# Optimization experiments

Measured on AMD Instinct MI355X. Metric: run time of the kernel, lower is better.

The kernel has to match this reference:

```python
import jax, jax.numpy as jnp
import numpy as np

MEM = 64  # memory_size from init_kwargs


def setup_inputs() -> dict:
    key = jax.random.key(0)
    ks = jax.random.split(key, 16)
    D, H, B, T = 128, 512, 512, 128
    n = lambda k, shape, s=0.02: jax.random.normal(k, shape, dtype=jnp.float32) * s
    # Gate order for stacked weights: [s, f, i, T, u, o]; Ws stacks [f, i, T, u, o].
    return {
        "X_seq": n(ks[0], (B, T, D + 1), 1.0),
        "Wh": n(ks[1], (6, H, H)), "bh_lin": jnp.zeros((6, H)),
        "Wx": n(ks[2], (6, D, H)), "bx_lin": jnp.zeros((6, H)),
        "Wst": n(ks[3], (1, H)), "bst": jnp.zeros((H,)),
        "Ws": n(ks[4], (5, H, H)), "bs_lin": jnp.zeros((5, H)),
        "bg": jnp.zeros((6, H)),
        "Waq": n(ks[5], (2 * H, H)), "baq": jnp.zeros((H,)),
        "Wah": n(ks[6], (H, H)), "bah": jnp.zeros((H,)),
        "vt": n(ks[7], (H, 1), 0.05),
        "W_h": n(ks[8], (H, H)), "b_Wh": jnp.zeros((H,)),
        "We": n(ks[9], (H, H)), "b_We": jnp.zeros((H,)),
        "Wg": n(ks[10], (D, H)), "b_Wg": jnp.zeros((H,)),
        "bh_p": jnp.zeros((H,)),
        "Wc": n(ks[11], (H, 1)), "bc": jnp.zeros((1,)),
    }


def reference(X_seq, Wh, bh_lin, Wx, bx_lin, Wst, bst, Ws, bs_lin, bg,
              Waq, baq, Wah, bah, vt, W_h, b_Wh, We, b_We, Wg, b_Wg, bh_p, Wc, bc):
    B, T, _ = X_seq.shape
    H = Wh.shape[-1]
    x_all = X_seq[:, :, :-1]          # [B, T, D]
    dt_all = X_seq[:, :, -1:]         # [B, T, 1]

    def step(carry, inp):
        h_prev, c_prev = carry
        x_t, d_t = inp                 # [B, D], [B, 1]
        # batched GEMMs over the 6 gates (s, f, i, T, u, o)
        pre_h = jnp.einsum('bh,ghk->gbk', h_prev, Wh) + bh_lin[:, None, :]
        pre_x = jnp.einsum('bd,gdk->gbk', x_t, Wx) + bx_lin[:, None, :]
        s_t = jnp.tanh(pre_h[0] + pre_x[0] + d_t @ Wst + bst + bg[0])
        pre_s = jnp.einsum('bh,ghk->gbk', s_t, Ws) + bs_lin[:, None, :]  # [f,i,T,u,o]
        f_t = jax.nn.sigmoid(pre_h[1] + pre_x[1] + pre_s[0] + bg[1])
        i_t = jax.nn.sigmoid(pre_h[2] + pre_x[2] + pre_s[1] + bg[2])
        T_t = jax.nn.sigmoid(pre_h[3] + pre_x[3] + pre_s[2] + bg[3])
        z_t = jnp.tanh(pre_h[4] + pre_x[4] + pre_s[3] + bg[4])
        c_t = f_t * c_prev + i_t * z_t + T_t * s_t
        o_t = jax.nn.sigmoid(pre_h[5] + pre_x[5] + pre_s[4] + bg[5])
        h_t = o_t * jnp.tanh(c_t)
        return (h_t, c_t), h_t

    h0 = jnp.zeros((B, H), dtype=X_seq.dtype)
    c0 = jnp.zeros((B, H), dtype=X_seq.dtype)
    xs = (jnp.swapaxes(x_all, 0, 1), jnp.swapaxes(dt_all, 0, 1))
    (h_last, c_last), h_tildes = jax.lax.scan(step, (h0, c0), xs)  # h_tildes: [T, B, H]

    # sliding window of last MEM hidden states (T >= MEM so all zeros are pushed out)
    hs = jnp.swapaxes(h_tildes[-MEM:], 0, 1)  # [B, MEM, H]

    q = jnp.concatenate([h_last, c_last], axis=1)                       # [B, 2H]
    o_att = jnp.tanh((q @ Waq + baq)[:, None, :] + hs @ Wah + bah)       # [B, MEM, H]
    alpha = jnp.exp((o_att @ vt)[..., 0])                                # [B, MEM] (matches torch exp/sum)
    alpha = alpha / jnp.sum(alpha, axis=1, keepdims=True)
    e_t = jnp.einsum('bm,bmh->bh', alpha, hs)
    h_fin = jnp.tanh(h_last @ W_h + b_Wh + e_t @ We + b_We
                     + x_all[:, -1] @ Wg + b_Wg + bh_p)
    return jax.nn.sigmoid(h_fin @ Wc + bc)  # [B, 1]
```

## Files before the change

### kernel.cpp

```cpp
#include <hip/hip_runtime.h>
#include <hip/hip_bf16.h>

typedef __bf16 bf16x8 __attribute__((ext_vector_type(8)));
typedef float f32x4 __attribute__((ext_vector_type(4)));

constexpr int NB   = 512;
constexpr int NT   = 128;
constexpr int ND   = 128;
constexpr int NH   = 512;
constexpr int NMEM = 64;
constexpr int KKA  = 640;
constexpr int KKB  = 1152;

constexpr int BAR_CNT = 0;
constexpr int BAR_GB  = 64;
constexpr int BAR_MFL = 8448;
constexpr int BAR_DFL = 12800;
constexpr int BAR_TOT = 16384;

__device__ __forceinline__ float sigm_(float x) { return 1.f / (1.f + expf(-x)); }

__device__ __forceinline__ unsigned ld_rlx_sys(const unsigned* p) {
    return __hip_atomic_load(p, __ATOMIC_RELAXED, __HIP_MEMORY_SCOPE_SYSTEM);
}
__device__ __forceinline__ unsigned ld_acq_sys(const unsigned* p) {
    return __hip_atomic_load(p, __ATOMIC_ACQUIRE, __HIP_MEMORY_SCOPE_SYSTEM);
}
__device__ __forceinline__ void st_rel_sys(unsigned* p, unsigned v) {
    __hip_atomic_store(p, v, __ATOMIC_RELEASE, __HIP_MEMORY_SCOPE_SYSTEM);
}
__device__ __forceinline__ unsigned ld_rlx_agt(const unsigned* p) {
    return __hip_atomic_load(p, __ATOMIC_RELAXED, __HIP_MEMORY_SCOPE_AGENT);
}
__device__ __forceinline__ unsigned ld_acq_agt(const unsigned* p) {
    return __hip_atomic_load(p, __ATOMIC_ACQUIRE, __HIP_MEMORY_SCOPE_AGENT);
}
__device__ __forceinline__ void st_rlx_agt(unsigned* p, unsigned v) {
    __hip_atomic_store(p, v, __ATOMIC_RELAXED, __HIP_MEMORY_SCOPE_AGENT);
}


__global__ void k_shufA(const float* __restrict__ Wh, const float* __restrict__ Wx,
                        __hip_bfloat16* __restrict__ WA_shuf) {
    int nb = blockIdx.x / 20, kk = blockIdx.x % 20;
    int lane = threadIdx.x;
    int n = nb * 16 + (lane & 15);
    int kbase = kk * 32 + (lane >> 4) * 8;
    size_t o = ((size_t)blockIdx.x * 64 + lane) * 8;
    for (int e = 0; e < 8; ++e) {
        int k = kbase + e;
        float v = (k < 512) ? Wh[(size_t)k * NH + n]
                            : Wx[(size_t)(k - 512) * NH + n];
        WA_shuf[o + e] = __float2bfloat16(v);
    }
}

__global__ void k_shufB(const float* __restrict__ Wh, const float* __restrict__ Wx,
                        const float* __restrict__ Ws, __hip_bfloat16* __restrict__ WB_shuf) {
    int idx = blockIdx.x;
    int kk = idx % 36, g = (idx / 36) % 5, jb = idx / 180;
    int lane = threadIdx.x;
    int j = jb * 16 + (lane & 15);
    int kbase = kk * 32 + (lane >> 4) * 8;
    size_t o = ((size_t)idx * 64 + lane) * 8;
    for (int e = 0; e < 8; ++e) {
        int k = kbase + e;
        float v;
        if (k < 512)      v = Wh[(size_t)(g + 1) * NH * NH + (size_t)k * NH + j];
        else if (k < 640) v = Wx[(size_t)(g + 1) * ND * NH + (size_t)(k - 512) * NH + j];
        else              v = Ws[(size_t)g * NH * NH + (size_t)(k - 640) * NH + j];
        WB_shuf[o + e] = __float2bfloat16(v);
    }
}

__global__ void k_shufW(const float* __restrict__ Wah, __hip_bfloat16* __restrict__ Wah_shuf) {
    int nb = blockIdx.x / 16, kk = blockIdx.x % 16;
    int lane = threadIdx.x;
    int j = nb * 16 + (lane & 15);
    int kbase = kk * 32 + (lane >> 4) * 8;
    size_t o = ((size_t)blockIdx.x * 64 + lane) * 8;
    for (int e = 0; e < 8; ++e)
        Wah_shuf[o + e] = __float2bfloat16(Wah[(size_t)(kbase + e) * NH + j]);
}

__global__ void k_biases(const float* bh_lin, const float* bx_lin, const float* bst,
                         const float* bs_lin, const float* bg,
                         const float* b_Wh, const float* b_We, const float* b_Wg, const float* bh_p,
                         float* bias_s, float* bias_g, float* bias_fin) {
    int j = threadIdx.x;
    bias_s[j] = bh_lin[j] + bx_lin[j] + bst[j] + bg[j];
    for (int g = 0; g < 5; ++g)
        bias_g[g * NH + j] = bh_lin[(g + 1) * NH + j] + bx_lin[(g + 1) * NH + j] +
                             bs_lin[g * NH + j] + bg[(g + 1) * NH + j];
    bias_fin[j] = b_Wh[j] + b_We[j] + b_Wg[j] + bh_p[j];
}

__global__ void k_init(const float* __restrict__ X_seq, float* __restrict__ Dt,
                       __hip_bfloat16* __restrict__ A_big, unsigned* __restrict__ bar) {
    int b = blockIdx.x, tid = threadIdx.x;
    if (b == 0) for (int i = tid; i < BAR_TOT; i += 256) bar[i] = 0;
    if (tid < NT) Dt[tid * NB + b] = X_seq[((size_t)b * NT + tid) * (ND + 1) + ND];
    for (int c = tid; c < KKB; c += 256) {
        float v = 0.f;
        if (c >= 512 && c < 640) v = X_seq[(size_t)b * NT * (ND + 1) + (c - 512)];
        A_big[(size_t)b * KKB + c] = __float2bfloat16(v);
    }
}

__device__ __forceinline__ void gbar2(unsigned* __restrict__ gb, int wg, unsigned gen) {
    __syncthreads();
    const int tid = threadIdx.x;
    if (tid == 0) st_rel_sys(&gb[wg * 32], gen);
    if (wg == 0) {
        while (ld_rlx_sys(&gb[tid * 32]) < gen) {}
        (void)ld_acq_sys(&gb[tid * 32]);
        __syncthreads();
        if (tid == 0) st_rel_sys(&gb[256 * 32], gen);
    }
    if (tid == 0) {
        while (ld_rlx_sys(&gb[256 * 32]) < gen) {}
        (void)ld_acq_sys(&gb[256 * 32]);
    }
    __syncthreads();
}

__device__ __forceinline__ void gbarL(unsigned* __restrict__ bar, unsigned xcd, unsigned rank,
                                      unsigned gen) {
    const int tid = threadIdx.x;
    __syncthreads();
    if (tid == 0) st_rlx_agt(&bar[BAR_MFL + (xcd * 32 + rank) * 16], gen);
    if (rank == 0) {
        if (tid < 32) { while (ld_rlx_agt(&bar[BAR_MFL + (xcd * 32 + tid) * 16]) < gen) {} }
        __syncthreads();
        if (tid == 0) st_rlx_agt(&bar[BAR_DFL + xcd * 32], gen);
    }
    if (tid == 0) {
        while (ld_rlx_agt(&bar[BAR_DFL + xcd * 32]) < gen) {}
        (void)ld_acq_agt(&bar[BAR_DFL + xcd * 32]);
    }
    __syncthreads();
}


__global__ __launch_bounds__(256, 1) void lstm_coop(
    const float* __restrict__ X_seq, const float* __restrict__ Dt,
    const __hip_bfloat16* __restrict__ WA_shuf, const __hip_bfloat16* __restrict__ WB_shuf,
    const float* __restrict__ bias_s, const float* __restrict__ bias_g,
    const float* __restrict__ Wst,
    __hip_bfloat16* __restrict__ A_big,
    float* __restrict__ c_last, float* __restrict__ s_f32, float* __restrict__ h_last,
    __hip_bfloat16* __restrict__ hist,
    unsigned* __restrict__ bar)
{
    const int wg = blockIdx.x;
    const int tid = threadIdx.x;
    const int wv = tid >> 6;
    const int lane = tid & 63;
    const int l15 = lane & 15, lhi = lane >> 4;

    __shared__ unsigned sh_meta[2];
    __shared__ unsigned sh_cnt[8];
    if (tid == 0) {
        unsigned xcc;
        asm volatile("s_getreg_b32 %0, hwreg(HW_REG_XCC_ID)" : "=s"(xcc));
        xcc &= 7u;
        unsigned r = __hip_atomic_fetch_add(&bar[BAR_CNT + xcc], 1u,
                                            __ATOMIC_RELAXED, __HIP_MEMORY_SCOPE_AGENT);
        sh_meta[0] = xcc; sh_meta[1] = r;
    }
    __syncthreads();
    gbar2(bar + BAR_GB, wg, 1u);
    if (tid < 8) sh_cnt[tid] = ld_rlx_sys(&bar[BAR_CNT + tid]);
    __syncthreads();
    bool local_ok = true;
    #pragma unroll
    for (int j = 0; j < 8; ++j) if (sh_cnt[j] != 32u) local_ok = false;

    const unsigned xcd  = local_ok ? sh_meta[0] : (unsigned)(wg & 7);
    const unsigned rank = local_ok ? sh_meta[1] : (unsigned)(wg >> 3);
    const int row_base  = (int)xcd * 64;

    const int colj = (int)rank * 16 + l15;

    const float ebs  = bias_s[colj];
    const float ewst = Wst[colj];
    float bgc[5];
    #pragma unroll
    for (int g = 0; g < 5; ++g) bgc[g] = bias_g[g * NH + colj];

    const __hip_bfloat16* wa_base = WA_shuf + (size_t)rank * 20 * 512 + lane * 8;
    const __hip_bfloat16* wb_base = WB_shuf + (size_t)rank * 5 * 36 * 512 + lane * 8;

    f32x4 c_reg = {0.f, 0.f, 0.f, 0.f};

    for (int t = 0; t < NT; ++t) {
        const int buf = t & 1;
        const __hip_bfloat16* A = A_big + (size_t)buf * NB * KKB;
        __hip_bfloat16* An = A_big + (size_t)(buf ^ 1) * NB * KKB;
        __hip_bfloat16* Aw = A_big + (size_t)buf * NB * KKB;

        {
            f32x4 acc = {0.f, 0.f, 0.f, 0.f};
            const __hip_bfloat16* arow = A + (size_t)(row_base + wv * 16 + l15) * KKB + lhi * 8;
            #pragma unroll 4
            for (int kk = 0; kk < 20; ++kk) {
                bf16x8 af = *reinterpret_cast<const bf16x8*>(arow + kk * 32);
                bf16x8 bfv = *reinterpret_cast<const bf16x8*>(wa_base + kk * 512);
                acc = __builtin_amdgcn_mfma_f32_16x16x32_bf16(af, bfv, acc, 0, 0, 0);
            }
            #pragma unroll
            for (int r = 0; r < 4; ++r) {
                int row = row_base + wv * 16 + lhi * 4 + r;
                float s = tanhf(acc[r] + ebs + Dt[t * NB + row] * ewst);
                s_f32[row * NH + colj] = s;
                Aw[(size_t)row * KKB + 640 + colj] = __float2bfloat16(s);
            }
        }
        if (local_ok) gbarL(bar, xcd, rank, (unsigned)(2 * t + 1));
        else          gbar2(bar + BAR_GB, wg, (unsigned)(2 * t + 2));

        {
            f32x4 acc[5] = {};
            const __hip_bfloat16* arow = A + (size_t)(row_base + wv * 16 + l15) * KKB + lhi * 8;
            for (int kk = 0; kk < 36; ++kk) {
                bf16x8 af = *reinterpret_cast<const bf16x8*>(arow + kk * 32);
                #pragma unroll
                for (int g = 0; g < 5; ++g) {
                    bf16x8 bfv = *reinterpret_cast<const bf16x8*>(wb_base + (g * 36 + kk) * 512);
                    acc[g] = __builtin_amdgcn_mfma_f32_16x16x32_bf16(af, bfv, acc[g], 0, 0, 0);
                }
            }
            #pragma unroll
            for (int r = 0; r < 4; ++r) {
                int row = row_base + wv * 16 + lhi * 4 + r;
                float f  = sigm_(acc[0][r] + bgc[0]);
                float i  = sigm_(acc[1][r] + bgc[1]);
                float Tg = sigm_(acc[2][r] + bgc[2]);
                float z  = tanhf(acc[3][r] + bgc[3]);
                float o  = sigm_(acc[4][r] + bgc[4]);
                float sv = s_f32[row * NH + colj];
                float cn = f * c_reg[r] + i * z + Tg * sv;
                c_reg[r] = cn;
                float hn = o * tanhf(cn);
                An[(size_t)row * KKB + colj] = __float2bfloat16(hn);
                if (t >= NT - NMEM)
                    hist[((size_t)(t - (NT - NMEM)) * NB + row) * NH + colj] = __float2bfloat16(hn);
                if (t == NT - 1) {
                    h_last[row * NH + colj] = hn;
                    c_last[row * NH + colj] = cn;
                }
            }
            if (t < NT - 1) {
                int idx = (int)rank * 256 + tid;
                int rr = idx >> 7, d = idx & 127;
                int row = row_base + rr;
                float xv = X_seq[((size_t)row * NT + (t + 1)) * (ND + 1) + d];
                An[(size_t)row * KKB + 512 + d] = __float2bfloat16(xv);
            }
        }
        if (local_ok) gbarL(bar, xcd, rank, (unsigned)(2 * t + 2));
        else          gbar2(bar + BAR_GB, wg, (unsigned)(2 * t + 3));
    }
}


__global__ void k_qa(const float* __restrict__ h_last, const float* __restrict__ c_last,
                     const float* __restrict__ Waq, const float* __restrict__ baq,
                     float* __restrict__ qa) {
    __shared__ float qs[8][1024];
    int b0 = blockIdx.x * 8;
    for (int idx = threadIdx.x; idx < 8 * 1024; idx += 512) {
        int bb = idx >> 10, k = idx & 1023;
        qs[bb][k] = (k < 512) ? h_last[(b0 + bb) * NH + k] : c_last[(b0 + bb) * NH + (k - 512)];
    }
    __syncthreads();
    int j = threadIdx.x;
    float acc[8] = {};
    for (int k = 0; k < 1024; ++k) {
        float w = Waq[(size_t)k * NH + j];
        #pragma unroll
        for (int bb = 0; bb < 8; ++bb) acc[bb] += qs[bb][k] * w;
    }
    float bq = baq[j];
    for (int bb = 0; bb < 8; ++bb) qa[(b0 + bb) * NH + j] = acc[bb] + bq;
}

__global__ void k_scores(const __hip_bfloat16* __restrict__ hist,
                         const __hip_bfloat16* __restrict__ Wah_shuf,
                         const float* __restrict__ qa, const float* __restrict__ bah,
                         const float* __restrict__ vt, float* __restrict__ score_part) {
    int rt = blockIdx.x, jt = blockIdx.y;
    int tid = threadIdx.x, wv = tid >> 6, lane = tid & 63;
    int l15 = lane & 15, lhi = lane >> 4;
    int R0 = rt * 64 + wv * 16;
    f32x4 acc[4] = {};
    const __hip_bfloat16* arow = hist + (size_t)(R0 + l15) * NH + lhi * 8;
    const __hip_bfloat16* bbase = Wah_shuf + lane * 8;
    for (int kk = 0; kk < 16; ++kk) {
        bf16x8 af = *reinterpret_cast<const bf16x8*>(arow + kk * 32);
        #pragma unroll
        for (int f = 0; f < 4; ++f) {
            int nb = jt * 4 + f;
            bf16x8 bfv = *reinterpret_cast<const bf16x8*>(bbase + (size_t)(nb * 16 + kk) * 512);
            acc[f] = __builtin_amdgcn_mfma_f32_16x16x32_bf16(af, bfv, acc[f], 0, 0, 0);
        }
    }
    float part[4] = {};
    #pragma unroll
    for (int r = 0; r < 4; ++r) {
        int R = R0 + lhi * 4 + r;
        int b = R & (NB - 1);
        #pragma unroll
        for (int f = 0; f < 4; ++f) {
            int j = (jt * 4 + f) * 16 + l15;
            float v = acc[f][r] + qa[b * NH + j] + bah[j];
            part[r] += tanhf(v) * vt[j];
        }
    }
    #pragma unroll
    for (int m = 1; m <= 8; m <<= 1)
        #pragma unroll
        for (int r = 0; r < 4; ++r) part[r] += __shfl_xor(part[r], m);
    if (l15 == 0)
        #pragma unroll
        for (int r = 0; r < 4; ++r)
            score_part[(size_t)jt * (NMEM * NB) + R0 + lhi * 4 + r] = part[r];
}

__global__ void k_softmax_e(const float* __restrict__ score_part,
                            const __hip_bfloat16* __restrict__ hist,
                            float* __restrict__ e_buf) {
    int b = blockIdx.x, m = threadIdx.x;
    float sc = 0.f;
    for (int p = 0; p < 8; ++p) sc += score_part[(size_t)p * (NMEM * NB) + m * NB + b];
    float mx = sc;
    for (int off = 32; off; off >>= 1) mx = fmaxf(mx, __shfl_xor(mx, off));
    float ex = expf(sc - mx);
    float sm = ex;
    for (int off = 32; off; off >>= 1) sm += __shfl_xor(sm, off);
    float alpha = ex / sm;
    __shared__ float al[64];
    al[m] = alpha;
    __syncthreads();
    for (int j0 = 0; j0 < NH; j0 += 64) {
        int j = j0 + m;
        float acc = 0.f;
        for (int mm = 0; mm < 64; ++mm)
            acc += al[mm] * __bfloat162float(hist[((size_t)mm * NB + b) * NH + j]);
        e_buf[b * NH + j] = acc;
    }
}

__global__ void k_final(const float* __restrict__ h_last, const float* __restrict__ e_buf,
                        const float* __restrict__ X_seq, const float* __restrict__ W_h,
                        const float* __restrict__ We, const float* __restrict__ Wg,
                        const float* __restrict__ bias_fin, float* __restrict__ h_fin) {
    __shared__ float hs[8][512], es[8][512], xs[8][128];
    int b0 = blockIdx.x * 8;
    for (int idx = threadIdx.x; idx < 8 * 512; idx += 512) {
        int bb = idx >> 9, k = idx & 511;
        hs[bb][k] = h_last[(b0 + bb) * NH + k];
        es[bb][k] = e_buf[(b0 + bb) * NH + k];
    }
    for (int idx = threadIdx.x; idx < 8 * 128; idx += 512) {
        int bb = idx >> 7, d = idx & 127;
        xs[bb][d] = X_seq[((size_t)(b0 + bb) * NT + (NT - 1)) * (ND + 1) + d];
    }
    __syncthreads();
    int j = threadIdx.x;
    float acc[8];
    float bfv = bias_fin[j];
    #pragma unroll
    for (int bb = 0; bb < 8; ++bb) acc[bb] = bfv;
    for (int k = 0; k < 512; ++k) {
        float w = W_h[(size_t)k * NH + j];
        #pragma unroll
        for (int bb = 0; bb < 8; ++bb) acc[bb] += hs[bb][k] * w;
    }
    for (int k = 0; k < 512; ++k) {
        float w = We[(size_t)k * NH + j];
        #pragma unroll
        for (int bb = 0; bb < 8; ++bb) acc[bb] += es[bb][k] * w;
    }
    for (int d = 0; d < 128; ++d) {
        float w = Wg[(size_t)d * NH + j];
        #pragma unroll
        for (int bb = 0; bb < 8; ++bb) acc[bb] += xs[bb][d] * w;
    }
    for (int bb = 0; bb < 8; ++bb) h_fin[(b0 + bb) * NH + j] = tanhf(acc[bb]);
}

__global__ void k_out(const float* __restrict__ h_fin, const float* __restrict__ Wc,
                      const float* __restrict__ bc, float* __restrict__ out) {
    int b = blockIdx.x, tid = threadIdx.x;
    float p = 0.f;
    for (int j = tid; j < NH; j += 256) p += h_fin[b * NH + j] * Wc[j];
    for (int off = 32; off; off >>= 1) p += __shfl_xor(p, off);
    __shared__ float red[4];
    if ((tid & 63) == 0) red[tid >> 6] = p;
    __syncthreads();
    if (tid == 0) out[b] = 1.f / (1.f + expf(-(red[0] + red[1] + red[2] + red[3] + bc[0])));
}


extern "C" void kernel_launch(void* const* d_in, const int* in_sizes, int n_in,
                              void* d_out, int out_size, void* d_ws, size_t ws_size,
                              hipStream_t stream) {
    const float* X_seq  = (const float*)d_in[0];
    const float* Wh     = (const float*)d_in[1];
    const float* bh_lin = (const float*)d_in[2];
    const float* Wx     = (const float*)d_in[3];
    const float* bx_lin = (const float*)d_in[4];
    const float* Wst    = (const float*)d_in[5];
    const float* bst    = (const float*)d_in[6];
    const float* Ws     = (const float*)d_in[7];
    const float* bs_lin = (const float*)d_in[8];
    const float* bg     = (const float*)d_in[9];
    const float* Waq    = (const float*)d_in[10];
    const float* baq    = (const float*)d_in[11];
    const float* Wah    = (const float*)d_in[12];
    const float* bah    = (const float*)d_in[13];
    const float* vt     = (const float*)d_in[14];
    const float* W_h    = (const float*)d_in[15];
    const float* b_Wh   = (const float*)d_in[16];
    const float* We     = (const float*)d_in[17];
    const float* b_We   = (const float*)d_in[18];
    const float* Wg     = (const float*)d_in[19];
    const float* b_Wg   = (const float*)d_in[20];
    const float* bh_p   = (const float*)d_in[21];
    const float* Wc     = (const float*)d_in[22];
    const float* bc     = (const float*)d_in[23];
    float* out = (float*)d_out;

    char* ws = (char*)d_ws;
    size_t off = 0;
    auto alloc = [&](size_t bytes) -> char* {
        char* p = ws + off;
        off = (off + bytes + 255) & ~(size_t)255;
        return p;
    };
    __hip_bfloat16* WA_shuf  = (__hip_bfloat16*)alloc((size_t)KKA * NH * 2);
    __hip_bfloat16* WB_shuf  = (__hip_bfloat16*)alloc((size_t)KKB * 5 * NH * 2);
    __hip_bfloat16* Wah_shuf = (__hip_bfloat16*)alloc((size_t)NH * NH * 2);
    float* bias_s   = (float*)alloc(NH * 4);
    float* bias_g   = (float*)alloc(5 * NH * 4);
    float* bias_fin = (float*)alloc(NH * 4);
    float* Dt       = (float*)alloc((size_t)NT * NB * 4);
    __hip_bfloat16* A_big = (__hip_bfloat16*)alloc((size_t)2 * NB * KKB * 2);
    float* c_last   = (float*)alloc((size_t)NB * NH * 4);
    float* s_f32    = (float*)alloc((size_t)NB * NH * 4);
    float* h_last   = (float*)alloc((size_t)NB * NH * 4);
    __hip_bfloat16* hist = (__hip_bfloat16*)alloc((size_t)NMEM * NB * NH * 2);
    float* qa       = (float*)alloc((size_t)NB * NH * 4);
    float* score_part = (float*)alloc((size_t)8 * NMEM * NB * 4);
    float* e_buf    = (float*)alloc((size_t)NB * NH * 4);
    float* h_fin    = (float*)alloc((size_t)NB * NH * 4);
    unsigned* bar   = (unsigned*)alloc((size_t)BAR_TOT * 4 + 4096);

    hipLaunchKernelGGL(k_shufA, dim3(32 * 20), dim3(64), 0, stream, Wh, Wx, WA_shuf);
    hipLaunchKernelGGL(k_shufB, dim3(32 * 5 * 36), dim3(64), 0, stream, Wh, Wx, Ws, WB_shuf);
    hipLaunchKernelGGL(k_shufW, dim3(32 * 16), dim3(64), 0, stream, Wah, Wah_shuf);
    hipLaunchKernelGGL(k_biases, dim3(1), dim3(512), 0, stream,
                       bh_lin, bx_lin, bst, bs_lin, bg, b_Wh, b_We, b_Wg, bh_p,
                       bias_s, bias_g, bias_fin);
    hipLaunchKernelGGL(k_init, dim3(NB), dim3(256), 0, stream, X_seq, Dt, A_big, bar);

    {
        void* args[] = {(void*)&X_seq, (void*)&Dt, (void*)&WA_shuf, (void*)&WB_shuf,
                        (void*)&bias_s, (void*)&bias_g, (void*)&Wst, (void*)&A_big,
                        (void*)&c_last, (void*)&s_f32, (void*)&h_last, (void*)&hist,
                        (void*)&bar};
        hipLaunchCooperativeKernel((void*)lstm_coop, dim3(256), dim3(256), args, 0, stream);
    }

    hipLaunchKernelGGL(k_qa, dim3(64), dim3(512), 0, stream, h_last, c_last, Waq, baq, qa);
    hipLaunchKernelGGL(k_scores, dim3(512, 8), dim3(256), 0, stream,
                       hist, Wah_shuf, qa, bah, vt, score_part);
    hipLaunchKernelGGL(k_softmax_e, dim3(NB), dim3(64), 0, stream, score_part, hist, e_buf);
    hipLaunchKernelGGL(k_final, dim3(64), dim3(512), 0, stream,
                       h_last, e_buf, X_seq, W_h, We, Wg, bias_fin, h_fin);
    hipLaunchKernelGGL(k_out, dim3(NB), dim3(256), 0, stream, h_fin, Wc, bc, out);
}
```

Before: 3.862 ms.

## Split gate GEMMs across two wave groups per block with LDS exchange

Doubles the cooperative LSTM block to 512 threads and splits the five gate GEMMs across two groups of four waves. One group computes z/o, the other f/i/T, and partial accumulators are exchanged through LDS. The next-step x load moves into the idle group during the s-gate phase. This cuts per-wave MFMA serial chain length on the recurrent critical path. The cost is an extra block-level sync per step, higher barrier cost with more threads, and some imbalance: group 0 does 2 gates plus s, group 1 does 3 gates.

```diff
diff --git a/kernel.cpp b/kernel.cpp
--- a/kernel.cpp
+++ b/kernel.cpp
@@ -112,8 +112,10 @@
     const int tid = threadIdx.x;
     if (tid == 0) st_rel_sys(&gb[wg * 32], gen);
     if (wg == 0) {
-        while (ld_rlx_sys(&gb[tid * 32]) < gen) {}
-        (void)ld_acq_sys(&gb[tid * 32]);
+        if (tid < 256) {
+            while (ld_rlx_sys(&gb[tid * 32]) < gen) {}
+            (void)ld_acq_sys(&gb[tid * 32]);
+        }
         __syncthreads();
         if (tid == 0) st_rel_sys(&gb[256 * 32], gen);
     }
@@ -142,7 +144,7 @@
 }
 
 
-__global__ __launch_bounds__(256, 1) void lstm_coop(
+__global__ __launch_bounds__(512, 1) void lstm_coop(
     const float* __restrict__ X_seq, const float* __restrict__ Dt,
     const __hip_bfloat16* __restrict__ WA_shuf, const __hip_bfloat16* __restrict__ WB_shuf,
     const float* __restrict__ bias_s, const float* __restrict__ bias_g,
@@ -157,6 +159,10 @@
     const int wv = tid >> 6;
     const int lane = tid & 63;
     const int l15 = lane & 15, lhi = lane >> 4;
+    const int rt  = wv & 3;
+    const int grp = wv >> 2;
+
+    __shared__ f32x4 lds_g[4][3][64];
 
     __shared__ unsigned sh_meta[2];
     __shared__ unsigned sh_cnt[8];
@@ -199,9 +205,9 @@
         __hip_bfloat16* An = A_big + (size_t)(buf ^ 1) * NB * KKB;
         __hip_bfloat16* Aw = A_big + (size_t)buf * NB * KKB;
 
-        {
+        if (grp == 0) {
             f32x4 acc = {0.f, 0.f, 0.f, 0.f};
-            const __hip_bfloat16* arow = A + (size_t)(row_base + wv * 16 + l15) * KKB + lhi * 8;
+            const __hip_bfloat16* arow = A + (size_t)(row_base + rt * 16 + l15) * KKB + lhi * 8;
             #pragma unroll 4
             for (int kk = 0; kk < 20; ++kk) {
                 bf16x8 af = *reinterpret_cast<const bf16x8*>(arow + kk * 32);
@@ -210,52 +216,66 @@
             }
             #pragma unroll
             for (int r = 0; r < 4; ++r) {
-                int row = row_base + wv * 16 + lhi * 4 + r;
+                int row = row_base + rt * 16 + lhi * 4 + r;
                 float s = tanhf(acc[r] + ebs + Dt[t * NB + row] * ewst);
                 s_f32[row * NH + colj] = s;
                 Aw[(size_t)row * KKB + 640 + colj] = __float2bfloat16(s);
             }
+        } else if (t < NT - 1) {
+            int idx = (int)rank * 256 + (tid - 256);
+            int rr = idx >> 7, d = idx & 127;
+            int row = row_base + rr;
+            float xv = X_seq[((size_t)row * NT + (t + 1)) * (ND + 1) + d];
+            An[(size_t)row * KKB + 512 + d] = __float2bfloat16(xv);
         }
         if (local_ok) gbarL(bar, xcd, rank, (unsigned)(2 * t + 1));
         else          gbar2(bar + BAR_GB, wg, (unsigned)(2 * t + 2));
 
         {
-            f32x4 acc[5] = {};
-            const __hip_bfloat16* arow = A + (size_t)(row_base + wv * 16 + l15) * KKB + lhi * 8;
+            f32x4 acc[3] = {};
+            const int g0 = (grp == 0) ? 3 : 0;
+            const int ng = (grp == 0) ? 2 : 3;
+            const __hip_bfloat16* arow = A + (size_t)(row_base + rt * 16 + l15) * KKB + lhi * 8;
             for (int kk = 0; kk < 36; ++kk) {
                 bf16x8 af = *reinterpret_cast<const bf16x8*>(arow + kk * 32);
                 #pragma unroll
-                for (int g = 0; g < 5; ++g) {
-                    bf16x8 bfv = *reinterpret_cast<const bf16x8*>(wb_base + (g * 36 + kk) * 512);
-                    acc[g] = __builtin_amdgcn_mfma_f32_16x16x32_bf16(af, bfv, acc[g], 0, 0, 0);
+                for (int gi = 0; gi < 3; ++gi) {
+                    if (gi < ng) {
+                        bf16x8 bfv = *reinterpret_cast<const bf16x8*>(
+                            wb_base + ((g0 + gi) * 36 + kk) * 512);
+                        acc[gi] = __builtin_amdgcn_mfma_f32_16x16x32_bf16(af, bfv, acc[gi], 0, 0, 0);
+                    }
                 }
             }
-            #pragma unroll
-            for (int r = 0; r < 4; ++r) {
-                int row = row_base + wv * 16 + lhi * 4 + r;
-                float f  = sigm_(acc[0][r] + bgc[0]);
-                float i  = sigm_(acc[1][r] + bgc[1]);
-                float Tg = sigm_(acc[2][r] + bgc[2]);
-                float z  = tanhf(acc[3][r] + bgc[3]);
-                float o  = sigm_(acc[4][r] + bgc[4]);
-                float sv = s_f32[row * NH + colj];
-                float cn = f * c_reg[r] + i * z + Tg * sv;
-                c_reg[r] = cn;
-                float hn = o * tanhf(cn);
-                An[(size_t)row * KKB + colj] = __float2bfloat16(hn);
-                if (t >= NT - NMEM)
-                    hist[((size_t)(t - (NT - NMEM)) * NB + row) * NH + colj] = __float2bfloat16(hn);
-                if (t == NT - 1) {
-                    h_last[row * NH + colj] = hn;
-                    c_last[row * NH + colj] = cn;
+            if (grp == 1) {
+                #pragma unroll
+                for (int gi = 0; gi < 3; ++gi) lds_g[rt][gi][lane] = acc[gi];
+            }
+            __syncthreads();
+            if (grp == 0) {
+                f32x4 a_f = lds_g[rt][0][lane];
+                f32x4 a_i = lds_g[rt][1][lane];
+                f32x4 a_T = lds_g[rt][2][lane];
+                #pragma unroll
+                for (int r = 0; r < 4; ++r) {
+                    int row = row_base + rt * 16 + lhi * 4 + r;
+                    float f  = sigm_(a_f[r] + bgc[0]);
+                    float i  = sigm_(a_i[r] + bgc[1]);
+                    float Tg = sigm_(a_T[r] + bgc[2]);
+                    float z  = tanhf(acc[0][r] + bgc[3]);
+                    float o  = sigm_(acc[1][r] + bgc[4]);
+                    float sv = s_f32[row * NH + colj];
+                    float cn = f * c_reg[r] + i * z + Tg * sv;
+                    c_reg[r] = cn;
+                    float hn = o * tanhf(cn);
+                    An[(size_t)row * KKB + colj] = __float2bfloat16(hn);
+                    if (t >= NT - NMEM)
+                        hist[((size_t)(t - (NT - NMEM)) * NB + row) * NH + colj] = __float2bfloat16(hn);
+                    if (t == NT - 1) {
+                        h_last[row * NH + colj] = hn;
+                        c_last[row * NH + colj] = cn;
+                    }
                 }
-            }
-            if (t < NT - 1) {
-                int idx = (int)rank * 256 + tid;
-                int rr = idx >> 7, d = idx & 127;
-                int row = row_base + rr;
-                float xv = X_seq[((size_t)row * NT + (t + 1)) * (ND + 1) + d];
-                An[(size_t)row * KKB + 512 + d] = __float2bfloat16(xv);
             }
         }
         if (local_ok) gbarL(bar, xcd, rank, (unsigned)(2 * t + 2));
@@ -470,7 +490,7 @@
                         (void*)&bias_s, (void*)&bias_g, (void*)&Wst, (void*)&A_big,
                         (void*)&c_last, (void*)&s_f32, (void*)&h_last, (void*)&hist,
                         (void*)&bar};
-        hipLaunchCooperativeKernel((void*)lstm_coop, dim3(256), dim3(256), args, 0, stream);
+        hipLaunchCooperativeKernel((void*)lstm_coop, dim3(256), dim3(512), args, 0, stream);
     }
 
     hipLaunchKernelGGL(k_qa, dim3(64), dim3(512), 0, stream, h_last, c_last, Waq, baq, qa);
```

Result: slower. 5.929 ms (+53.5%).
